# Kernel tuning notes

Measured on AMD Instinct MI355X. Metric: run time of the kernel, lower is better.

## Reference

```python
import jax, jax.numpy as jnp
import numpy as np

B, N = 8, 2048
CLIP, D, BD, NC = 512, 256, 128, 10  # CLIP_EMBED_DIM, GNN_NODE_DIM, BOTTLENECK_DIM_GNN, NUM_CLASSES
LN_EPS = 1e-5


def _layer_norm(x, g, b):
    mu = jnp.mean(x, axis=-1, keepdims=True)
    var = jnp.mean(jnp.square(x - mu), axis=-1, keepdims=True)
    return (x - mu) / jnp.sqrt(var + LN_EPS) * g + b


def setup_inputs() -> dict:
    key = jax.random.key(0)
    ks = jax.random.split(key, 16)
    def w(k, shape, fan_in):
        lim = 1.0 / np.sqrt(fan_in)
        return jax.random.uniform(k, shape, jnp.float32, -lim, lim)
    return {
        "local_feat": jax.random.normal(ks[0], (B, N, CLIP), jnp.float32),
        "coords": jax.random.uniform(ks[1], (B, N, 2), jnp.float32),
        "mask": jax.random.randint(ks[2], (B, N), 0, 2).astype(bool),
        # node_encoder: Linear(CLIP->D) + LayerNorm(D)
        "enc_w": w(ks[3], (CLIP, D), CLIP), "enc_b": jnp.zeros((D,), jnp.float32),
        "enc_g": jnp.ones((D,), jnp.float32), "enc_beta": jnp.zeros((D,), jnp.float32),
        "gamma": jnp.asarray(5.0, jnp.float32),  # spatial_gamma
        "wq": w(ks[4], (D, D), D), "bq": jnp.zeros((D,), jnp.float32),
        "wk": w(ks[5], (D, D), D), "bk": jnp.zeros((D,), jnp.float32),
        "wv": w(ks[6], (D, D), D), "bv": jnp.zeros((D,), jnp.float32),
        # bottleneck: Linear(D->BD) + LayerNorm(BD)
        "bn_w": w(ks[7], (D, BD), D), "bn_b": jnp.zeros((BD,), jnp.float32),
        "bn_g": jnp.ones((BD,), jnp.float32), "bn_beta": jnp.zeros((BD,), jnp.float32),
        # classifier: Linear(BD->BD//2) + ReLU + Linear(BD//2->NC)
        "c1_w": w(ks[8], (BD, BD // 2), BD), "c1_b": jnp.zeros((BD // 2,), jnp.float32),
        "c2_w": w(ks[9], (BD // 2, NC), BD // 2), "c2_b": jnp.zeros((NC,), jnp.float32),
    }


def reference(local_feat, coords, mask, enc_w, enc_b, enc_g, enc_beta, gamma,
              wq, bq, wk, bk, wv, bv, bn_w, bn_b, bn_g, bn_beta,
              c1_w, c1_b, c2_w, c2_b):
    # node encoder: Linear + LN + ReLU -> h [B,N,D]
    h = jax.nn.relu(_layer_norm(local_feat @ enc_w + enc_b, enc_g, enc_beta))
    # pairwise euclidean distances on 2D coords (torch.cdist, under no_grad)
    xy = coords[:, :, :2]
    sq = jnp.sum(xy * xy, axis=-1)                                   # [B,N]
    d2 = sq[:, :, None] + sq[:, None, :] - 2.0 * jnp.einsum('bnd,bmd->bnm', xy, xy)
    dist = jax.lax.stop_gradient(jnp.sqrt(jnp.maximum(d2, 0.0)))     # [B,N,N]
    spatial_adj = jnp.exp(-dist * jnp.abs(gamma))
    q, k, v = h @ wq + bq, h @ wk + bk, h @ wv + bv
    scores = jnp.einsum('bnd,bmd->bnm', q, k) / jnp.sqrt(jnp.float32(D))
    attn = jax.nn.softmax(scores, axis=-1) * spatial_adj             # gated attention
    attn = jnp.where(mask[:, None, :], 0.0, attn)                    # zero masked keys
    agg = jnp.einsum('bnm,bmd->bnd', attn, v)                        # [B,N,D]
    out = jax.nn.relu(_layer_norm(agg @ bn_w + bn_b, bn_g, bn_beta)) # [B,N,BD]
    mask_v = (~mask)[:, :, None].astype(out.dtype)                   # [B,N,1]
    pooled = (out * mask_v).sum(axis=1) / jnp.maximum(mask_v.sum(axis=1), 1e-9)
    logits = jax.nn.relu(pooled @ c1_w + c1_b) @ c2_w + c2_b
    return logits, pooled
```

## Files before the change

kernel.cpp:

```cpp
#include <hip/hip_runtime.h>
#include <hip/hip_bf16.h>

typedef unsigned short ushort_t;
typedef __attribute__((ext_vector_type(8))) short s8;
typedef __attribute__((ext_vector_type(4))) float f4;

__device__ __forceinline__ unsigned short f2bf(float f) {
  union { float f; unsigned int u; } c; c.f = f;
  unsigned int r = (c.u + 0x7fffu + ((c.u >> 16) & 1u)) >> 16;
  return (unsigned short)r;
}
__device__ __forceinline__ float bf2f(ushort_t u) {
  union { unsigned int i; float f; } c; c.i = ((unsigned int)u) << 16; return c.f;
}
__device__ __forceinline__ uint4 pack8(float4 a, float4 b) {
  uint4 r;
  r.x = (unsigned)f2bf(a.x) | ((unsigned)f2bf(a.y) << 16);
  r.y = (unsigned)f2bf(a.z) | ((unsigned)f2bf(a.w) << 16);
  r.z = (unsigned)f2bf(b.x) | ((unsigned)f2bf(b.y) << 16);
  r.w = (unsigned)f2bf(b.z) | ((unsigned)f2bf(b.w) << 16);
  return r;
}
__device__ __forceinline__ float fsqrt_fast(float x) {
  float r; asm("v_sqrt_f32 %0, %1" : "=v"(r) : "v"(x)); return r;
}
__device__ __forceinline__ float fexp2_fast(float x) {
  float r; asm("v_exp_f32 %0, %1" : "=v"(r) : "v"(x)); return r;
}
__device__ __forceinline__ void dma16(const ushort_t* g, const short* l) {
  __builtin_amdgcn_global_load_lds(
      (const __attribute__((address_space(1))) unsigned int*)g,
      (__attribute__((address_space(3))) unsigned int*)(unsigned long)l,
      16, 0, 0);
}

#define LOG2E 1.44269504f

__global__ __launch_bounds__(256) void k_wt_all(
    const float* __restrict__ enc_w, const float* __restrict__ wq,
    const float* __restrict__ wk, const float* __restrict__ wv,
    const float* __restrict__ bn_w,
    ushort_t* __restrict__ enc_wT, ushort_t* __restrict__ wqkvT,
    ushort_t* __restrict__ bn_wT) {
  const int y = blockIdx.y;
  const int i = blockIdx.x * 256 + threadIdx.x;
  if (y == 0) {
    if (i < 131072) { const int n = i >> 9, k = i & 511; enc_wT[i] = f2bf(enc_w[k * 256 + n]); }
  } else if (y <= 3) {
    if (i < 65536) {
      const int n = i >> 8, k = i & 255;
      const float* src = (y == 1) ? wq : (y == 2) ? wk : wv;
      wqkvT[(y - 1) * 65536 + i] = f2bf(src[k * 256 + n]);
    }
  } else {
    if (i < 32768) { const int n = i >> 8, k = i & 255; bn_wT[i] = f2bf(bn_w[k * 128 + n]); }
  }
}

__global__ __launch_bounds__(256, 3) void k_gemm_enc(
    const float* __restrict__ A, const ushort_t* __restrict__ WT,
    const float* __restrict__ bia, const float* __restrict__ g,
    const float* __restrict__ beta, ushort_t* __restrict__ out) {
  __shared__ short Al[32 * 72];
  __shared__ short Bl[256 * 72];
  __shared__ float red1[32][2], red2[32][2];
  const int t = threadIdx.x;
  const int wv = t >> 6, lane = t & 63, l16 = lane & 15, quad = lane >> 4;
  const int wm = wv >> 1, wn = wv & 1;
  const int row0 = blockIdx.x * 32;

  f4 acc[8];
#pragma unroll
  for (int nf = 0; nf < 8; ++nf) acc[nf] = (f4){0.f, 0.f, 0.f, 0.f};

  for (int k0 = 0; k0 < 512; k0 += 64) {
    __syncthreads();
    {
      const int r = t >> 3, c8 = t & 7;
      const float* src = &A[(size_t)(row0 + r) * 512 + k0 + c8 * 8];
      *(uint4*)&Al[r * 72 + c8 * 8] =
          pack8(*(const float4*)src, *(const float4*)(src + 4));
    }
#pragma unroll
    for (int i = 0; i < 8; ++i) {
      const int ch = t + i * 256;
      const int r = ch >> 3, c8 = ch & 7;
      *(uint4*)&Bl[r * 72 + c8 * 8] =
          *(const uint4*)&WT[(size_t)r * 512 + k0 + c8 * 8];
    }
    __syncthreads();
#pragma unroll
    for (int kc = 0; kc < 2; ++kc) {
      const s8 af = *(const s8*)&Al[(wm * 16 + l16) * 72 + kc * 32 + quad * 8];
#pragma unroll
      for (int nf = 0; nf < 8; ++nf) {
        const s8 bf = *(const s8*)&Bl[(wn * 128 + nf * 16 + l16) * 72 + kc * 32 + quad * 8];
        acc[nf] = __builtin_amdgcn_mfma_f32_16x16x32_bf16(af, bf, acc[nf], 0, 0, 0);
      }
    }
  }
  float bi[8], gg[8], bb[8];
#pragma unroll
  for (int nf = 0; nf < 8; ++nf) {
    const int col = wn * 128 + nf * 16 + l16;
    bi[nf] = bia[col]; gg[nf] = g[col]; bb[nf] = beta[col];
  }
  float s1[4] = {0.f, 0.f, 0.f, 0.f}, s2[4] = {0.f, 0.f, 0.f, 0.f};
#pragma unroll
  for (int nf = 0; nf < 8; ++nf)
#pragma unroll
    for (int r = 0; r < 4; ++r) {
      const float v = acc[nf][r] + bi[nf];
      acc[nf][r] = v;
      s1[r] += v; s2[r] += v * v;
    }
#pragma unroll
  for (int m = 1; m < 16; m <<= 1) {
#pragma unroll
    for (int r = 0; r < 4; ++r) {
      s1[r] += __shfl_xor(s1[r], m);
      s2[r] += __shfl_xor(s2[r], m);
    }
  }
  if (l16 == 0) {
#pragma unroll
    for (int r = 0; r < 4; ++r) {
      const int rl = wm * 16 + quad * 4 + r;
      red1[rl][wn] = s1[r]; red2[rl][wn] = s2[r];
    }
  }
  __syncthreads();
#pragma unroll
  for (int r = 0; r < 4; ++r) {
    const int rl = wm * 16 + quad * 4 + r;
    const float mu = (red1[rl][0] + red1[rl][1]) * (1.f / 256.f);
    const float var = (red2[rl][0] + red2[rl][1]) * (1.f / 256.f) - mu * mu;
    const float rstd = rsqrtf(var + 1e-5f);
#pragma unroll
    for (int nf = 0; nf < 8; ++nf) {
      const int col = wn * 128 + nf * 16 + l16;
      const float v = (acc[nf][r] - mu) * rstd * gg[nf] + bb[nf];
      out[(size_t)(row0 + rl) * 256 + col] = f2bf(fmaxf(v, 0.f));
    }
  }
}

__global__ __launch_bounds__(256, 4) void k_gemm_qkv(
    const ushort_t* __restrict__ A, const ushort_t* __restrict__ WT,
    const float* __restrict__ bq, const float* __restrict__ bk,
    const float* __restrict__ bv,
    ushort_t* __restrict__ q, ushort_t* __restrict__ k, ushort_t* __restrict__ vt) {
  __shared__ short Al[64 * 72];
  __shared__ short Bl[128 * 72];
  const int t = threadIdx.x;
  const int wv = t >> 6, lane = t & 63, l16 = lane & 15, quad = lane >> 4;
  const int wm = wv >> 1, wn = wv & 1;
  const int row0 = blockIdx.x * 64;
  const int nb = blockIdx.y;
  const int type = nb >> 1;
  const ushort_t* wtb = WT + (size_t)nb * 128 * 256;

  f4 acc[2][4];
#pragma unroll
  for (int mf = 0; mf < 2; ++mf)
#pragma unroll
    for (int nf = 0; nf < 4; ++nf) acc[mf][nf] = (f4){0.f, 0.f, 0.f, 0.f};

  for (int k0 = 0; k0 < 256; k0 += 64) {
    __syncthreads();
#pragma unroll
    for (int i = 0; i < 2; ++i) {
      const int ch = t + i * 256;
      const int r = ch >> 3, c8 = ch & 7;
      *(uint4*)&Al[r * 72 + c8 * 8] =
          *(const uint4*)&A[(size_t)(row0 + r) * 256 + k0 + c8 * 8];
    }
#pragma unroll
    for (int i = 0; i < 4; ++i) {
      const int ch = t + i * 256;
      const int r = ch >> 3, c8 = ch & 7;
      *(uint4*)&Bl[r * 72 + c8 * 8] =
          *(const uint4*)&wtb[(size_t)r * 256 + k0 + c8 * 8];
    }
    __syncthreads();
#pragma unroll
    for (int kc = 0; kc < 2; ++kc) {
      s8 af[2];
      af[0] = *(const s8*)&Al[(wm * 32 + l16) * 72 + kc * 32 + quad * 8];
      af[1] = *(const s8*)&Al[(wm * 32 + 16 + l16) * 72 + kc * 32 + quad * 8];
#pragma unroll
      for (int nf = 0; nf < 4; ++nf) {
        const s8 bf = *(const s8*)&Bl[(wn * 64 + nf * 16 + l16) * 72 + kc * 32 + quad * 8];
        acc[0][nf] = __builtin_amdgcn_mfma_f32_16x16x32_bf16(af[0], bf, acc[0][nf], 0, 0, 0);
        acc[1][nf] = __builtin_amdgcn_mfma_f32_16x16x32_bf16(af[1], bf, acc[1][nf], 0, 0, 0);
      }
    }
  }
  const float* bias = (type == 0) ? bq : (type == 1) ? bk : bv;
#pragma unroll
  for (int nf = 0; nf < 4; ++nf) {
    const int colg = nb * 128 + wn * 64 + nf * 16 + l16;
    const int col = colg - type * 256;
    const float bi = bias[col];
    if (type == 2) {
      const int b = row0 >> 11;
#pragma unroll
      for (int mf = 0; mf < 2; ++mf) {
        const int n = (row0 & 2047) + wm * 32 + quad * 8 + mf * 4;
        ushort4 pk;
        pk.x = f2bf(acc[mf][nf][0] + bi);
        pk.y = f2bf(acc[mf][nf][1] + bi);
        pk.z = f2bf(acc[mf][nf][2] + bi);
        pk.w = f2bf(acc[mf][nf][3] + bi);
        *(ushort4*)&vt[((size_t)b * 256 + col) * 2048 + n] = pk;
      }
    } else {
      ushort_t* dst = (type == 0) ? q : k;
      const float sc = (type == 0) ? (0.0625f * LOG2E) : 1.f;
#pragma unroll
      for (int mf = 0; mf < 2; ++mf)
#pragma unroll
        for (int r = 0; r < 4; ++r) {
          const int row = row0 + wm * 32 + mf * 16 + quad * 4 + r;
          dst[(size_t)row * 256 + col] = f2bf((acc[mf][nf][r] + bi) * sc);
        }
    }
  }
}

__global__ __launch_bounds__(512, 4) void k_attn(
    const ushort_t* __restrict__ qb, const ushort_t* __restrict__ kb,
    const ushort_t* __restrict__ vtb,
    const float* __restrict__ coords, const int* __restrict__ mask,
    const float* __restrict__ gam,
    ushort_t* __restrict__ Opb, float* __restrict__ lws) {
  __shared__ short kld[2][8192];
  __shared__ short vld[2][8192];
  __shared__ __align__(16) float2 cls[512];
  __shared__ __align__(16) float  mls[512];
  const int t = threadIdx.x;
  const int wv = t >> 6, lane = t & 63, l16 = lane & 15, quad = lane >> 4;
  const int b = blockIdx.z, ks = blockIdx.y;
  const int qw = blockIdx.x * 128 + wv * 16;
  const int kbase = ks * 512;

  const ushort_t* kbb = kb + ((size_t)b * 2048 + kbase) * 256;
  const ushort_t* vbb = vtb + (size_t)b * 256 * 2048 + kbase;

  {
    const int key = t & 31, dg = t >> 5;
    dma16(kbb + (size_t)key * 256 + dg * 8, &kld[0][t * 8]);
    dma16(kbb + (size_t)key * 256 + dg * 8 + 128, &kld[0][(t + 512) * 8]);
    const int d = t & 255, kg = t >> 8;
    dma16(vbb + (size_t)d * 2048 + kg * 8, &vld[0][t * 8]);
    dma16(vbb + (size_t)d * 2048 + kg * 8 + 16, &vld[0][(t + 512) * 8]);
  }
  cls[t] = ((const float2*)coords)[b * 2048 + kbase + t];
  mls[t] = mask[b * 2048 + kbase + t] ? 0.f : 1.f;

  s8 qa[8];
  {
    const ushort_t* qrow = qb + ((size_t)b * 2048 + qw + l16) * 256 + quad * 8;
#pragma unroll
    for (int c = 0; c < 8; ++c) qa[c] = *(const s8*)(qrow + c * 32);
  }
  float rcx, rcy;
  {
    const float2 cc = ((const float2*)coords)[b * 2048 + qw + l16];
    rcx = cc.x; rcy = cc.y;
  }
  const float gl2 = fabsf(gam[0]) * LOG2E;

  f4 o[16];
#pragma unroll
  for (int dt = 0; dt < 16; ++dt) o[dt] = (f4){0.f, 0.f, 0.f, 0.f};
  float lrun = 0.f;

  __syncthreads();

  for (int kt = 0; kt < 16; ++kt) {
    const int cur = kt & 1;

    if (kt < 15) {
      const ushort_t* kn = kbb + (size_t)(kt + 1) * 8192;
      const ushort_t* vn = vbb + (kt + 1) * 32;
      const int nb2 = cur ^ 1;
      const int key = t & 31, dg = t >> 5;
      dma16(kn + (size_t)key * 256 + dg * 8, &kld[nb2][t * 8]);
      dma16(kn + (size_t)key * 256 + dg * 8 + 128, &kld[nb2][(t + 512) * 8]);
      const int d = t & 255, kg = t >> 8;
      dma16(vn + (size_t)d * 2048 + kg * 8, &vld[nb2][t * 8]);
      dma16(vn + (size_t)d * 2048 + kg * 8 + 16, &vld[nb2][(t + 512) * 8]);
    }

    f4 sc[2];
    sc[0] = (f4){0.f, 0.f, 0.f, 0.f};
    sc[1] = (f4){0.f, 0.f, 0.f, 0.f};
#pragma unroll
    for (int c = 0; c < 8; ++c) {
      const s8 kf0 = *(const s8*)&kld[cur][((c * 4 + quad) * 32 + l16) * 8];
      sc[0] = __builtin_amdgcn_mfma_f32_16x16x32_bf16(kf0, qa[c], sc[0], 0, 0, 0);
      const s8 kf1 = *(const s8*)&kld[cur][((c * 4 + quad) * 32 + 16 + l16) * 8];
      sc[1] = __builtin_amdgcn_mfma_f32_16x16x32_bf16(kf1, qa[c], sc[1], 0, 0, 0);
    }

    unsigned pu[4];
#pragma unroll
    for (int s = 0; s < 2; ++s) {
      const int k0 = kt * 32 + s * 16 + quad * 4;
      const float4 c01 = *(const float4*)&cls[k0];
      const float4 c23 = *(const float4*)&cls[k0 + 2];
      const float4 mm = *(const float4*)&mls[k0];
      const float kx[4] = {c01.x, c01.z, c23.x, c23.z};
      const float ky[4] = {c01.y, c01.w, c23.y, c23.w};
      const float mv[4] = {mm.x, mm.y, mm.z, mm.w};
      float w[4];
#pragma unroll
      for (int r = 0; r < 4; ++r) {
        const float p = fexp2_fast(sc[s][r]);
        lrun += p;
        const float dx = rcx - kx[r], dy = rcy - ky[r];
        const float dist = fsqrt_fast(dx * dx + dy * dy);
        w[r] = p * fexp2_fast(-gl2 * dist) * mv[r];
      }
      pu[s * 2 + 0] = (unsigned)f2bf(w[0]) | ((unsigned)f2bf(w[1]) << 16);
      pu[s * 2 + 1] = (unsigned)f2bf(w[2]) | ((unsigned)f2bf(w[3]) << 16);
    }
    union { s8 v; unsigned u[4]; } cv;
    cv.u[0] = pu[0]; cv.u[1] = pu[1]; cv.u[2] = pu[2]; cv.u[3] = pu[3];
    const s8 paf = cv.v;

#pragma unroll
    for (int dt = 0; dt < 16; ++dt) {
      const s8 bvf = *(const s8*)&vld[cur][(quad * 256 + dt * 16 + l16) * 8];
      o[dt] = __builtin_amdgcn_mfma_f32_16x16x32_bf16(paf, bvf, o[dt], 0, 0, 0);
    }
    __syncthreads();
  }

  ushort_t* OpK = Opb + (size_t)ks * 4194304;
#pragma unroll
  for (int dt = 0; dt < 16; ++dt)
#pragma unroll
    for (int r = 0; r < 4; ++r)
      OpK[((size_t)b * 2048 + qw + quad * 4 + r) * 256 + dt * 16 + l16] =
          f2bf(o[dt][r]);

  lrun += __shfl_xor(lrun, 16);
  lrun += __shfl_xor(lrun, 32);
  if (quad == 0) lws[ks * 16384 + b * 2048 + qw + l16] = lrun;
}

__global__ __launch_bounds__(256, 3) void k_gemm_bn(
    const ushort_t* __restrict__ Opb, const float* __restrict__ lws,
    const ushort_t* __restrict__ WT,
    const float* __restrict__ bia, const float* __restrict__ g,
    const float* __restrict__ beta, float* __restrict__ pooledAcc) {
  __shared__ short Al[32 * 72];
  __shared__ short Bl[128 * 72];
  __shared__ float red1[32][2], red2[32][2];
  __shared__ float sCm[32];
  const int t = threadIdx.x;
  const int wv = t >> 6, lane = t & 63, l16 = lane & 15, quad = lane >> 4;
  const int wm = wv >> 1, wn = wv & 1;
  const int row0 = blockIdx.x * 32;
  const int b = row0 >> 11;

  if (t < 32) {
    const int row = row0 + t;
    sCm[t] = 1.f / (lws[row] + lws[16384 + row] + lws[32768 + row] + lws[49152 + row]);
  }

  f4 acc[4];
#pragma unroll
  for (int nf = 0; nf < 4; ++nf) acc[nf] = (f4){0.f, 0.f, 0.f, 0.f};

  for (int k0 = 0; k0 < 256; k0 += 64) {
    __syncthreads();
    {
      const int r = t >> 3, c8 = t & 7;
      const float c0 = sCm[r];
      const size_t off = (size_t)(row0 + r) * 256 + k0 + c8 * 8;
      float e[8];
#pragma unroll
      for (int j = 0; j < 8; ++j) e[j] = 0.f;
#pragma unroll
      for (int pp = 0; pp < 4; ++pp) {
        const uint4 u = *(const uint4*)&Opb[(size_t)pp * 4194304 + off];
        e[0] += bf2f((ushort_t)(u.x & 0xffff)); e[1] += bf2f((ushort_t)(u.x >> 16));
        e[2] += bf2f((ushort_t)(u.y & 0xffff)); e[3] += bf2f((ushort_t)(u.y >> 16));
        e[4] += bf2f((ushort_t)(u.z & 0xffff)); e[5] += bf2f((ushort_t)(u.z >> 16));
        e[6] += bf2f((ushort_t)(u.w & 0xffff)); e[7] += bf2f((ushort_t)(u.w >> 16));
      }
      float4 ea = {c0 * e[0], c0 * e[1], c0 * e[2], c0 * e[3]};
      float4 eb = {c0 * e[4], c0 * e[5], c0 * e[6], c0 * e[7]};
      *(uint4*)&Al[r * 72 + c8 * 8] = pack8(ea, eb);
    }
#pragma unroll
    for (int i = 0; i < 4; ++i) {
      const int ch = t + i * 256;
      const int r = ch >> 3, c8 = ch & 7;
      *(uint4*)&Bl[r * 72 + c8 * 8] =
          *(const uint4*)&WT[(size_t)r * 256 + k0 + c8 * 8];
    }
    __syncthreads();
#pragma unroll
    for (int kc = 0; kc < 2; ++kc) {
      const s8 af = *(const s8*)&Al[(wm * 16 + l16) * 72 + kc * 32 + quad * 8];
#pragma unroll
      for (int nf = 0; nf < 4; ++nf) {
        const s8 bf = *(const s8*)&Bl[(wn * 64 + nf * 16 + l16) * 72 + kc * 32 + quad * 8];
        acc[nf] = __builtin_amdgcn_mfma_f32_16x16x32_bf16(af, bf, acc[nf], 0, 0, 0);
      }
    }
  }
  float bi[4], gg[4], bb[4];
#pragma unroll
  for (int nf = 0; nf < 4; ++nf) {
    const int col = wn * 64 + nf * 16 + l16;
    bi[nf] = bia[col]; gg[nf] = g[col]; bb[nf] = beta[col];
  }
  float s1[4] = {0.f, 0.f, 0.f, 0.f}, s2[4] = {0.f, 0.f, 0.f, 0.f};
#pragma unroll
  for (int nf = 0; nf < 4; ++nf)
#pragma unroll
    for (int r = 0; r < 4; ++r) {
      const float v = acc[nf][r] + bi[nf];
      acc[nf][r] = v;
      s1[r] += v; s2[r] += v * v;
    }
#pragma unroll
  for (int m = 1; m < 16; m <<= 1) {
#pragma unroll
    for (int r = 0; r < 4; ++r) {
      s1[r] += __shfl_xor(s1[r], m);
      s2[r] += __shfl_xor(s2[r], m);
    }
  }
  if (l16 == 0) {
#pragma unroll
    for (int r = 0; r < 4; ++r) {
      const int rl = wm * 16 + quad * 4 + r;
      red1[rl][wn] = s1[r]; red2[rl][wn] = s2[r];
    }
  }
  __syncthreads();
#pragma unroll
  for (int r = 0; r < 4; ++r) {
    const int rl = wm * 16 + quad * 4 + r;
    const float mu = (red1[rl][0] + red1[rl][1]) * (1.f / 128.f);
    const float var = (red2[rl][0] + red2[rl][1]) * (1.f / 128.f) - mu * mu;
    const float rstd = rsqrtf(var + 1e-5f);
#pragma unroll
    for (int nf = 0; nf < 4; ++nf) {
      const float v = (acc[nf][r] - mu) * rstd * gg[nf] + bb[nf];
      acc[nf][r] = fmaxf(v, 0.f);
    }
  }
  {
    float mw[4];
#pragma unroll
    for (int r = 0; r < 4; ++r) {
      const int rl = wm * 16 + quad * 4 + r;
      mw[r] = pooledAcc[1024 + row0 + rl];
    }
#pragma unroll
    for (int nf = 0; nf < 4; ++nf) {
      float s = acc[nf][0] * mw[0] + acc[nf][1] * mw[1] +
                acc[nf][2] * mw[2] + acc[nf][3] * mw[3];
      s += __shfl_xor(s, 16);
      s += __shfl_xor(s, 32);
      if (quad == 0) {
        const int col = wn * 64 + nf * 16 + l16;
        atomicAdd(&pooledAcc[b * 128 + col], s);
      }
    }
  }
}

__global__ __launch_bounds__(256) void k_maskf(const int* __restrict__ mask,
                                               float* __restrict__ pooledAcc) {
  const int i = blockIdx.x * 256 + threadIdx.x;
  if (i < 16384) pooledAcc[1024 + i] = mask[i] ? 0.f : 1.f;
  if (i < 1024) pooledAcc[i] = 0.f;
}

__global__ __launch_bounds__(128) void k_pool2_head(
    const float* __restrict__ pooledAcc, const int* __restrict__ mask,
    const float* __restrict__ c1w, const float* __restrict__ c1b,
    const float* __restrict__ c2w, const float* __restrict__ c2b,
    float* __restrict__ dout) {
  __shared__ float ps[128];
  __shared__ float h1[64];
  __shared__ float scnt[128];
  const int b = blockIdx.x, t = threadIdx.x;
  float c = 0.f;
  const int* mb = mask + b * 2048 + t * 16;
#pragma unroll
  for (int j = 0; j < 16; ++j) c += mb[j] ? 0.f : 1.f;
  scnt[t] = c;
  __syncthreads();
  for (int o2 = 64; o2 > 0; o2 >>= 1) {
    if (t < o2) scnt[t] += scnt[t + o2];
    __syncthreads();
  }
  const float cnt = scnt[0];
  const float p = pooledAcc[b * 128 + t] / fmaxf(cnt, 1e-9f);
  ps[t] = p;
  dout[80 + b * 128 + t] = p;
  __syncthreads();
  if (t < 64) {
    float acc = c1b[t];
    for (int d = 0; d < 128; ++d) acc += ps[d] * c1w[d * 64 + t];
    h1[t] = fmaxf(acc, 0.f);
  }
  __syncthreads();
  if (t < 10) {
    float a2 = c2b[t];
    for (int j = 0; j < 64; ++j) a2 += h1[j] * c2w[j * 10 + t];
    dout[b * 10 + t] = a2;
  }
}

extern "C" void kernel_launch(void* const* d_in, const int* in_sizes, int n_in,
                              void* d_out, int out_size, void* d_ws, size_t ws_size,
                              hipStream_t stream) {
  const float* lf     = (const float*)d_in[0];
  const float* coords = (const float*)d_in[1];
  const int*   mask   = (const int*)d_in[2];
  const float* enc_w  = (const float*)d_in[3];
  const float* enc_b  = (const float*)d_in[4];
  const float* enc_g  = (const float*)d_in[5];
  const float* enc_be = (const float*)d_in[6];
  const float* gamma  = (const float*)d_in[7];
  const float* wq     = (const float*)d_in[8];
  const float* bq     = (const float*)d_in[9];
  const float* wk     = (const float*)d_in[10];
  const float* bk     = (const float*)d_in[11];
  const float* wv     = (const float*)d_in[12];
  const float* bv     = (const float*)d_in[13];
  const float* bn_w   = (const float*)d_in[14];
  const float* bn_b   = (const float*)d_in[15];
  const float* bn_g   = (const float*)d_in[16];
  const float* bn_be  = (const float*)d_in[17];
  const float* c1w    = (const float*)d_in[18];
  const float* c1b    = (const float*)d_in[19];
  const float* c2w    = (const float*)d_in[20];
  const float* c2b    = (const float*)d_in[21];

  float* ws = (float*)d_ws;
  ushort_t* h_bf   = (ushort_t*)ws;
  ushort_t* q_bf   = (ushort_t*)(ws + 2097152);
  ushort_t* k_bf   = (ushort_t*)(ws + 4194304);
  ushort_t* vt_bf  = (ushort_t*)(ws + 6291456);
  ushort_t* Opb    = (ushort_t*)(ws + 8388608);
  ushort_t* enc_wT = (ushort_t*)(ws + 17825792);
  ushort_t* wqkvT  = (ushort_t*)(ws + 17891328);
  ushort_t* bn_wT  = (ushort_t*)(ws + 17989632);
  float*    lws    = ws + 18006016;
  float*    pooledAcc = ws + 18071552;
  float* out = (float*)d_out;

  k_wt_all<<<dim3(512, 5), 256, 0, stream>>>(enc_w, wq, wk, wv, bn_w,
                                             enc_wT, wqkvT, bn_wT);
  k_maskf<<<64, 256, 0, stream>>>(mask, pooledAcc);
  k_gemm_enc<<<512, 256, 0, stream>>>(lf, enc_wT, enc_b, enc_g, enc_be, h_bf);
  k_gemm_qkv<<<dim3(256, 6), 256, 0, stream>>>(h_bf, wqkvT, bq, bk, bv, q_bf, k_bf, vt_bf);
  k_attn<<<dim3(16, 4, 8), 512, 0, stream>>>(q_bf, k_bf, vt_bf, coords, mask, gamma,
                                             Opb, lws);
  k_gemm_bn<<<512, 256, 0, stream>>>(Opb, lws, bn_wT, bn_b, bn_g, bn_be, pooledAcc);
  k_pool2_head<<<8, 128, 0, stream>>>(pooledAcc, mask, c1w, c1b, c2w, c2b, out);
}
```

Before: 220.1 us.

## Process two query tiles per wave in attention kernel to reuse K/V fragments

Each wave in the attention kernel now handles 32 query rows (two 16-row tiles) instead of 16, so every K and V fragment read from shared memory feeds two MFMAs. The grid is halved along the query dimension and launch bounds drop to 2 blocks per CU to make room for the doubled accumulators. This cuts LDS traffic and K/V tile loads per query, but raises register pressure, lowers occupancy, and leaves fewer blocks (256) to spread across the CUs.

```diff
diff --git a/kernel.cpp b/kernel.cpp
--- a/kernel.cpp
+++ b/kernel.cpp
@@ -228,7 +228,7 @@
   }
 }
 
-__global__ __launch_bounds__(512, 4) void k_attn(
+__global__ __launch_bounds__(512, 2) void k_attn(
     const ushort_t* __restrict__ qb, const ushort_t* __restrict__ kb,
     const ushort_t* __restrict__ vtb,
     const float* __restrict__ coords, const int* __restrict__ mask,
@@ -241,7 +241,7 @@
   const int t = threadIdx.x;
   const int wv = t >> 6, lane = t & 63, l16 = lane & 15, quad = lane >> 4;
   const int b = blockIdx.z, ks = blockIdx.y;
-  const int qw = blockIdx.x * 128 + wv * 16;
+  const int qw = blockIdx.x * 256 + wv * 32;
   const int kbase = ks * 512;
 
   const ushort_t* kbb = kb + ((size_t)b * 2048 + kbase) * 256;
@@ -258,23 +258,29 @@
   cls[t] = ((const float2*)coords)[b * 2048 + kbase + t];
   mls[t] = mask[b * 2048 + kbase + t] ? 0.f : 1.f;
 
-  s8 qa[8];
+  s8 qa[2][8];
   {
     const ushort_t* qrow = qb + ((size_t)b * 2048 + qw + l16) * 256 + quad * 8;
 #pragma unroll
-    for (int c = 0; c < 8; ++c) qa[c] = *(const s8*)(qrow + c * 32);
-  }
-  float rcx, rcy;
+    for (int c = 0; c < 8; ++c) {
+      qa[0][c] = *(const s8*)(qrow + c * 32);
+      qa[1][c] = *(const s8*)(qrow + 16 * 256 + c * 32);
+    }
+  }
+  float rcx[2], rcy[2];
   {
-    const float2 cc = ((const float2*)coords)[b * 2048 + qw + l16];
-    rcx = cc.x; rcy = cc.y;
+    const float2 c0 = ((const float2*)coords)[b * 2048 + qw + l16];
+    const float2 c1 = ((const float2*)coords)[b * 2048 + qw + 16 + l16];
+    rcx[0] = c0.x; rcy[0] = c0.y; rcx[1] = c1.x; rcy[1] = c1.y;
   }
   const float gl2 = fabsf(gam[0]) * LOG2E;
 
-  f4 o[16];
-#pragma unroll
-  for (int dt = 0; dt < 16; ++dt) o[dt] = (f4){0.f, 0.f, 0.f, 0.f};
-  float lrun = 0.f;
+  f4 o[2][16];
+#pragma unroll
+  for (int h = 0; h < 2; ++h)
+#pragma unroll
+    for (int dt = 0; dt < 16; ++dt) o[h][dt] = (f4){0.f, 0.f, 0.f, 0.f};
+  float lrun[2] = {0.f, 0.f};
 
   __syncthreads();
 
@@ -293,62 +299,77 @@
       dma16(vn + (size_t)d * 2048 + kg * 8 + 16, &vld[nb2][(t + 512) * 8]);
     }
 
-    f4 sc[2];
-    sc[0] = (f4){0.f, 0.f, 0.f, 0.f};
-    sc[1] = (f4){0.f, 0.f, 0.f, 0.f};
+    f4 sc[2][2];
+    sc[0][0] = (f4){0.f, 0.f, 0.f, 0.f}; sc[0][1] = (f4){0.f, 0.f, 0.f, 0.f};
+    sc[1][0] = (f4){0.f, 0.f, 0.f, 0.f}; sc[1][1] = (f4){0.f, 0.f, 0.f, 0.f};
 #pragma unroll
     for (int c = 0; c < 8; ++c) {
       const s8 kf0 = *(const s8*)&kld[cur][((c * 4 + quad) * 32 + l16) * 8];
-      sc[0] = __builtin_amdgcn_mfma_f32_16x16x32_bf16(kf0, qa[c], sc[0], 0, 0, 0);
+      sc[0][0] = __builtin_amdgcn_mfma_f32_16x16x32_bf16(kf0, qa[0][c], sc[0][0], 0, 0, 0);
+      sc[1][0] = __builtin_amdgcn_mfma_f32_16x16x32_bf16(kf0, qa[1][c], sc[1][0], 0, 0, 0);
       const s8 kf1 = *(const s8*)&kld[cur][((c * 4 + quad) * 32 + 16 + l16) * 8];
-      sc[1] = __builtin_amdgcn_mfma_f32_16x16x32_bf16(kf1, qa[c], sc[1], 0, 0, 0);
-    }
-
-    unsigned pu[4];
-#pragma unroll
-    for (int s = 0; s < 2; ++s) {
-      const int k0 = kt * 32 + s * 16 + quad * 4;
-      const float4 c01 = *(const float4*)&cls[k0];
-      const float4 c23 = *(const float4*)&cls[k0 + 2];
-      const float4 mm = *(const float4*)&mls[k0];
-      const float kx[4] = {c01.x, c01.z, c23.x, c23.z};
-      const float ky[4] = {c01.y, c01.w, c23.y, c23.w};
-      const float mv[4] = {mm.x, mm.y, mm.z, mm.w};
-      float w[4];
-#pragma unroll
-      for (int r = 0; r < 4; ++r) {
-        const float p = fexp2_fast(sc[s][r]);
-        lrun += p;
-        const float dx = rcx - kx[r], dy = rcy - ky[r];
-        const float dist = fsqrt_fast(dx * dx + dy * dy);
-        w[r] = p * fexp2_fast(-gl2 * dist) * mv[r];
-      }
-      pu[s * 2 + 0] = (unsigned)f2bf(w[0]) | ((unsigned)f2bf(w[1]) << 16);
-      pu[s * 2 + 1] = (unsigned)f2bf(w[2]) | ((unsigned)f2bf(w[3]) << 16);
-    }
-    union { s8 v; unsigned u[4]; } cv;
-    cv.u[0] = pu[0]; cv.u[1] = pu[1]; cv.u[2] = pu[2]; cv.u[3] = pu[3];
-    const s8 paf = cv.v;
+      sc[0][1] = __builtin_amdgcn_mfma_f32_16x16x32_bf16(kf1, qa[0][c], sc[0][1], 0, 0, 0);
+      sc[1][1] = __builtin_amdgcn_mfma_f32_16x16x32_bf16(kf1, qa[1][c], sc[1][1], 0, 0, 0);
+    }
+
+    s8 paf[2];
+#pragma unroll
+    for (int h = 0; h < 2; ++h) {
+      unsigned pu[4];
+#pragma unroll
+      for (int s = 0; s < 2; ++s) {
+        const int k0 = kt * 32 + s * 16 + quad * 4;
+        const float4 c01 = *(const float4*)&cls[k0];
+        const float4 c23 = *(const float4*)&cls[k0 + 2];
+        const float4 mm = *(const float4*)&mls[k0];
+        const float kx[4] = {c01.x, c01.z, c23.x, c23.z};
+        const float ky[4] = {c01.y, c01.w, c23.y, c23.w};
+        const float mv[4] = {mm.x, mm.y, mm.z, mm.w};
+        float w[4];
+#pragma unroll
+        for (int r = 0; r < 4; ++r) {
+          const float p = fexp2_fast(sc[h][s][r]);
+          lrun[h] += p;
+          const float dx = rcx[h] - kx[r], dy = rcy[h] - ky[r];
+          const float dist = fsqrt_fast(dx * dx + dy * dy);
+          w[r] = p * fexp2_fast(-gl2 * dist) * mv[r];
+        }
+        pu[s * 2 + 0] = (unsigned)f2bf(w[0]) | ((unsigned)f2bf(w[1]) << 16);
+        pu[s * 2 + 1] = (unsigned)f2bf(w[2]) | ((unsigned)f2bf(w[3]) << 16);
+      }
+      union { s8 v; unsigned u[4]; } cv;
+      cv.u[0] = pu[0]; cv.u[1] = pu[1]; cv.u[2] = pu[2]; cv.u[3] = pu[3];
+      paf[h] = cv.v;
+    }
 
 #pragma unroll
     for (int dt = 0; dt < 16; ++dt) {
       const s8 bvf = *(const s8*)&vld[cur][(quad * 256 + dt * 16 + l16) * 8];
-      o[dt] = __builtin_amdgcn_mfma_f32_16x16x32_bf16(paf, bvf, o[dt], 0, 0, 0);
+      o[0][dt] = __builtin_amdgcn_mfma_f32_16x16x32_bf16(paf[0], bvf, o[0][dt], 0, 0, 0);
+      o[1][dt] = __builtin_amdgcn_mfma_f32_16x16x32_bf16(paf[1], bvf, o[1][dt], 0, 0, 0);
     }
     __syncthreads();
   }
 
   ushort_t* OpK = Opb + (size_t)ks * 4194304;
 #pragma unroll
-  for (int dt = 0; dt < 16; ++dt)
-#pragma unroll
-    for (int r = 0; r < 4; ++r)
-      OpK[((size_t)b * 2048 + qw + quad * 4 + r) * 256 + dt * 16 + l16] =
-          f2bf(o[dt][r]);
-
-  lrun += __shfl_xor(lrun, 16);
-  lrun += __shfl_xor(lrun, 32);
-  if (quad == 0) lws[ks * 16384 + b * 2048 + qw + l16] = lrun;
+  for (int h = 0; h < 2; ++h)
+#pragma unroll
+    for (int dt = 0; dt < 16; ++dt)
+#pragma unroll
+      for (int r = 0; r < 4; ++r)
+        OpK[((size_t)b * 2048 + qw + h * 16 + quad * 4 + r) * 256 + dt * 16 + l16] =
+            f2bf(o[h][dt][r]);
+
+#pragma unroll
+  for (int h = 0; h < 2; ++h) {
+    lrun[h] += __shfl_xor(lrun[h], 16);
+    lrun[h] += __shfl_xor(lrun[h], 32);
+  }
+  if (quad == 0) {
+    lws[ks * 16384 + b * 2048 + qw + l16] = lrun[0];
+    lws[ks * 16384 + b * 2048 + qw + 16 + l16] = lrun[1];
+  }
 }
 
 __global__ __launch_bounds__(256, 3) void k_gemm_bn(
@@ -566,8 +587,8 @@
   k_maskf<<<64, 256, 0, stream>>>(mask, pooledAcc);
   k_gemm_enc<<<512, 256, 0, stream>>>(lf, enc_wT, enc_b, enc_g, enc_be, h_bf);
   k_gemm_qkv<<<dim3(256, 6), 256, 0, stream>>>(h_bf, wqkvT, bq, bk, bv, q_bf, k_bf, vt_bf);
-  k_attn<<<dim3(16, 4, 8), 512, 0, stream>>>(q_bf, k_bf, vt_bf, coords, mask, gamma,
-                                             Opb, lws);
+  k_attn<<<dim3(8, 4, 8), 512, 0, stream>>>(q_bf, k_bf, vt_bf, coords, mask, gamma,
+                                            Opb, lws);
   k_gemm_bn<<<512, 256, 0, stream>>>(Opb, lws, bn_wT, bn_b, bn_g, bn_be, pooledAcc);
   k_pool2_head<<<8, 128, 0, stream>>>(pooledAcc, mask, c1w, c1b, c2w, c2b, out);
 }
```

Result: slower. 225.5 us (+2.5%).
